# Kernel tuning notes

Hardware: AMD Instinct MI355X
Metric: run time of the kernel (lower is better)

The kernel has to match this reference:

```python
import jax, jax.numpy as jnp
import numpy as np

N_NODES = 100000


def gcn_conv(x, src, dst, ew, W, b, n_nodes):
    """PyG-style GCNConv: add self-loops, symmetric degree normalization,
    linear transform, scatter-add aggregation, bias."""
    loop = jnp.arange(n_nodes)
    src_f = jnp.concatenate([src, loop])          # [E+N]
    dst_f = jnp.concatenate([dst, loop])          # [E+N]
    ew_f = jnp.concatenate([ew, jnp.ones((n_nodes,), dtype=ew.dtype)])
    deg = jax.ops.segment_sum(ew_f, dst_f, num_segments=n_nodes)  # [N]
    dinv = jnp.where(deg > 0, jax.lax.rsqrt(deg), 0.0)
    norm = dinv[src_f] * ew_f * dinv[dst_f]       # [E+N]
    h = x @ W.T                                   # [N, out]
    msg = h[src_f] * norm[:, None]                # [E+N, out] gather + scale
    out = jax.ops.segment_sum(msg, dst_f, num_segments=n_nodes)
    return out + b


def prelu(x, a):
    return jnp.where(x >= 0, x, a * x)


def setup_inputs() -> dict:
    key = jax.random.key(0)
    k = jax.random.split(key, 8)
    in_c, out_c = 256, 128
    n_edges = 1600000
    x = jax.random.normal(k[0], (N_NODES, in_c), dtype=jnp.float32)
    edge_index = jax.random.randint(k[1], (2, n_edges), 0, N_NODES, dtype=jnp.int64)
    edge_weight = jax.random.uniform(k[2], (n_edges,), dtype=jnp.float32)
    W1 = jax.random.normal(k[3], (out_c, in_c), dtype=jnp.float32) / np.sqrt(in_c)
    b1 = jnp.zeros((out_c,), dtype=jnp.float32)
    W2 = jax.random.normal(k[4], (out_c, out_c), dtype=jnp.float32) / np.sqrt(out_c)
    b2 = jnp.zeros((out_c,), dtype=jnp.float32)
    a = jnp.asarray(0.25, dtype=jnp.float32)  # PReLU single shared parameter
    return {"x": x, "edge_index": edge_index, "edge_weight": edge_weight,
            "W1": W1, "b1": b1, "W2": W2, "b2": b2, "a": a}


def reference(x, edge_index, edge_weight, W1, b1, W2, b2, a):
    src, dst = edge_index[0], edge_index[1]
    h1 = prelu(gcn_conv(x, src, dst, edge_weight, W1, b1, N_NODES), a)
    h2 = prelu(gcn_conv(h1, src, dst, edge_weight, W2, b2, N_NODES), a)
    return (h1, h2)
```

## Files before the change

kernel.cpp:

```cpp
#include <hip/hip_runtime.h>


static __device__ __forceinline__ float4 ld4(const float* p) { return *(const float4*)p; }

static __device__ __forceinline__ unsigned short f2bf(float f) {
    unsigned u = __float_as_uint(f);
    u += 0x7fff + ((u >> 16) & 1);
    return (unsigned short)(u >> 16);
}
static __device__ __forceinline__ float bf2f(unsigned short h) {
    return __uint_as_float(((unsigned)h) << 16);
}

typedef __attribute__((ext_vector_type(8))) short short8v;
typedef __attribute__((ext_vector_type(4))) float f32x4;

static __device__ __forceinline__ int eidx(const void* ei, int flag, long long idx) {
    if (flag) return (int)((const long long*)ei)[idx];
    return ((const int*)ei)[idx];
}

#define CNT_SH 24
#define DEG_SCALE 262144.0f
#define DEG_INV   3.814697265625e-06f

__global__ void k_detect(const int* ei, int* flag) {
    __shared__ int anynz;
    if (threadIdx.x == 0) anynz = 0;
    __syncthreads();
    if (ei[2 * threadIdx.x + 1] != 0) anynz = 1;
    __syncthreads();
    if (threadIdx.x == 0) *flag = (anynz == 0) ? 1 : 0;
}

static __device__ __forceinline__ void packW_body(const float* __restrict__ W,
                                                  unsigned short* __restrict__ Bp,
                                                  int t, int kbits) {
    int K = 1 << kbits;
    int col = t >> kbits, k = t & (K - 1);
    int nt = col >> 4, ks = k >> 5;
    int lane = (col & 15) | (((k >> 3) & 3) << 4);
    int j = k & 7;
    Bp[((((size_t)nt * (K >> 5) + ks) * 64 + lane) << 3) + j] = f2bf(W[t]);
}

__global__ __launch_bounds__(256) void k_prep(unsigned* __restrict__ packed, int N,
                                              const float* __restrict__ W1,
                                              unsigned short* __restrict__ bp1,
                                              const float* __restrict__ W2,
                                              unsigned short* __restrict__ bp2,
                                              int nbInit) {
    int b = blockIdx.x;
    if (b < nbInit) {
        int i = b * 256 + threadIdx.x;
        if (i < N) packed[i] = 0u;
    } else if (b < nbInit + 128) {
        int t = (b - nbInit) * 256 + threadIdx.x;
        packW_body(W1, bp1, t, 8);
    } else {
        int t = (b - nbInit - 128) * 256 + threadIdx.x;
        packW_body(W2, bp2, t, 7);
    }
}

static __device__ __forceinline__ void count_body(const void* __restrict__ ei,
                                                  const float* __restrict__ ew,
                                                  int flag,
                                                  unsigned* __restrict__ packed,
                                                  int* __restrict__ rank,
                                                  int E, int cbid) {
    int base = cbid * 2048 + threadIdx.x;
    int d[8]; unsigned inc[8];
    #pragma unroll
    for (int u = 0; u < 8; ++u) {
        int e = base + u * 256;
        bool ok = e < E;
        int ec = ok ? e : 0;
        d[u]   = eidx(ei, flag, (long long)E + ec);
        inc[u] = ok ? ((1u << CNT_SH) | (unsigned)(ew[ec] * DEG_SCALE)) : 0u;
    }
    unsigned old[8];
    #pragma unroll
    for (int u = 0; u < 8; ++u)
        old[u] = atomicAdd(&packed[d[u]], inc[u]);
    __builtin_amdgcn_sched_barrier(0);
    #pragma unroll
    for (int u = 0; u < 8; ++u) {
        int e = base + u * 256;
        if (e < E) rank[e] = (int)(old[u] >> CNT_SH);
    }
}

template <int K>
static __device__ __forceinline__ void gemm_body(const float* __restrict__ X,
                                                 const unsigned short* __restrict__ Bp,
                                                 unsigned short* __restrict__ Hb,
                                                 int M, int gbid) {
    constexpr int KS = K / 32;
    int wave = threadIdx.x >> 6, lane = threadIdx.x & 63;
    int row0 = gbid * 128 + wave * 32;
    int r0 = row0 + (lane & 15);      if (r0 >= M) r0 = M - 1;
    int r1 = row0 + 16 + (lane & 15); if (r1 >= M) r1 = M - 1;
    int kc = (lane >> 4) * 8;
    const float* x0 = X + (size_t)r0 * K + kc;
    const float* x1 = X + (size_t)r1 * K + kc;

    f32x4 acc[2][8] = {};
    #pragma unroll 2
    for (int ks = 0; ks < KS; ++ks) {
        float4 a0 = ld4(x0 + ks * 32), a1 = ld4(x0 + ks * 32 + 4);
        float4 c0 = ld4(x1 + ks * 32), c1 = ld4(x1 + ks * 32 + 4);
        short8v af0, af1;
        af0[0] = (short)f2bf(a0.x); af0[1] = (short)f2bf(a0.y);
        af0[2] = (short)f2bf(a0.z); af0[3] = (short)f2bf(a0.w);
        af0[4] = (short)f2bf(a1.x); af0[5] = (short)f2bf(a1.y);
        af0[6] = (short)f2bf(a1.z); af0[7] = (short)f2bf(a1.w);
        af1[0] = (short)f2bf(c0.x); af1[1] = (short)f2bf(c0.y);
        af1[2] = (short)f2bf(c0.z); af1[3] = (short)f2bf(c0.w);
        af1[4] = (short)f2bf(c1.x); af1[5] = (short)f2bf(c1.y);
        af1[6] = (short)f2bf(c1.z); af1[7] = (short)f2bf(c1.w);
        #pragma unroll
        for (int nt = 0; nt < 8; ++nt) {
            short8v bf = *(const short8v*)&Bp[(((size_t)nt * KS + ks) * 64 + lane) * 8];
            acc[0][nt] = __builtin_amdgcn_mfma_f32_16x16x32_bf16(af0, bf, acc[0][nt], 0, 0, 0);
            acc[1][nt] = __builtin_amdgcn_mfma_f32_16x16x32_bf16(af1, bf, acc[1][nt], 0, 0, 0);
        }
    }
    #pragma unroll
    for (int rg = 0; rg < 2; ++rg) {
        int orow0 = row0 + rg * 16 + (lane >> 4) * 4;
        #pragma unroll
        for (int nt = 0; nt < 8; ++nt) {
            int col = nt * 16 + (lane & 15);
            #pragma unroll
            for (int j = 0; j < 4; ++j) {
                int r = orow0 + j;
                if (r < M) Hb[(size_t)r * 128 + col] = f2bf(acc[rg][nt][j]);
            }
        }
    }
}

__global__ __launch_bounds__(256) void k_count_gemm1(
        const void* __restrict__ ei, const float* __restrict__ ew,
        const int* __restrict__ flagp, unsigned* __restrict__ packed,
        int* __restrict__ rank, int E,
        const float* __restrict__ X, const unsigned short* __restrict__ Bp,
        unsigned short* __restrict__ Hb, int M, int nbCount) {
    int b = blockIdx.x;
    if (b < nbCount) {
        count_body(ei, ew, *flagp, packed, rank, E, b);
    } else {
        gemm_body<256>(X, Bp, Hb, M, b - nbCount);
    }
}

__global__ __launch_bounds__(256) void k_gemm2(const float* __restrict__ X,
                                               const unsigned short* __restrict__ Bp,
                                               unsigned short* __restrict__ Hb, int M) {
    gemm_body<128>(X, Bp, Hb, M, blockIdx.x);
}

__global__ __launch_bounds__(256) void k_blocksum(const unsigned* packed,
                                                  int* bsum, int N) {
    int i = blockIdx.x * 256 + threadIdx.x;
    int v = i < N ? (int)(packed[i] >> CNT_SH) : 0;
    for (int d = 32; d > 0; d >>= 1) v += __shfl_down(v, d, 64);
    __shared__ int wsum[4];
    int lane = threadIdx.x & 63, wid = threadIdx.x >> 6;
    if (lane == 0) wsum[wid] = v;
    __syncthreads();
    if (threadIdx.x == 0) bsum[blockIdx.x] = wsum[0] + wsum[1] + wsum[2] + wsum[3];
}

__global__ __launch_bounds__(512) void k_scan_bsum(int* bsum, int nb) {
    int t = threadIdx.x;
    int v = (t < nb) ? bsum[t] : 0;
    int orig = v;
    int lane = t & 63, wid = t >> 6;
    for (int d = 1; d < 64; d <<= 1) { int n = __shfl_up(v, d, 64); if (lane >= d) v += n; }
    __shared__ int wsum[8];
    if (lane == 63) wsum[wid] = v;
    __syncthreads();
    int woff = 0;
    for (int w = 0; w < 8; ++w) if (w < wid) woff += wsum[w];
    if (t < nb) bsum[t] = v - orig + woff;
}

__global__ __launch_bounds__(256) void k_scan_final(const unsigned* packed,
                                                    const int* bsum,
                                                    int* offs, float* dinv,
                                                    int N, int E) {
    int b = blockIdx.x, t = threadIdx.x;
    int i = b * 256 + t;
    unsigned pk = (i < N) ? packed[i] : 0u;
    int v = (int)(pk >> CNT_SH);
    int orig = v;
    int lane = t & 63, wid = t >> 6;
    for (int d = 1; d < 64; d <<= 1) { int n = __shfl_up(v, d, 64); if (lane >= d) v += n; }
    __shared__ int wsum[4];
    if (lane == 63) wsum[wid] = v;
    __syncthreads();
    int woff = bsum[b];
    for (int w = 0; w < 4; ++w) if (w < wid) woff += wsum[w];
    if (i < N) {
        offs[i] = v - orig + woff;
        float dg = 1.0f + (float)(pk & 0xFFFFFFu) * DEG_INV;
        dinv[i] = rsqrtf(dg);
    }
    if (i == 0) offs[N] = E;
}

__global__ __launch_bounds__(256) void k_scatter(const void* __restrict__ ei,
                                                 const float* __restrict__ ew,
                                                 const int* __restrict__ flagp,
                                                 const float* __restrict__ dinv,
                                                 const int* __restrict__ offs,
                                                 const int* __restrict__ rank,
                                                 int2* __restrict__ spair, int E) {
    const int flag = *flagp;
    int e = blockIdx.x * 256 + threadIdx.x;
    if (e < E) {
        int s = eidx(ei, flag, e);
        int d = eidx(ei, flag, (long long)E + e);
        int p = offs[d] + rank[e];
        float nrm = dinv[s] * ew[e] * dinv[d];
        int2 v; v.x = s; v.y = __float_as_int(nrm);
        spair[p] = v;
    }
}

__global__ __launch_bounds__(256) void k_agg(const unsigned short* __restrict__ Hb,
                                             const int* __restrict__ offs,
                                             const int2* __restrict__ spair,
                                             const float* __restrict__ dinv,
                                             const float* __restrict__ bias,
                                             const float* __restrict__ a_ptr,
                                             float* __restrict__ Out, int N) {
    int g = blockIdx.x * 8 + (threadIdx.x >> 5);
    int lane = threadIdx.x & 31;
    if (g >= N) return;
    float alpha = a_ptr[0];
    float di = dinv[g];
    float4 acc = ld4(bias + lane * 4);
    ushort4 hv = *(const ushort4*)(Hb + (size_t)g * 128 + lane * 4);
    float sw = di * di;
    acc.x += bf2f(hv.x) * sw; acc.y += bf2f(hv.y) * sw;
    acc.z += bf2f(hv.z) * sw; acc.w += bf2f(hv.w) * sw;
    int j0 = offs[g], j1 = offs[g + 1];
    for (int jb = j0; jb < j1; jb += 32) {
        int j = jb + lane;
        int s = 0; float w = 0.f;
        if (j < j1) { int2 sp = spair[j]; s = sp.x; w = __int_as_float(sp.y); }
        int cnt = j1 - jb; if (cnt > 32) cnt = 32;
        int full = cnt & ~3, i = 0;
        for (; i < full; i += 4) {
            int   s0 = __shfl(s, i,     32), s1 = __shfl(s, i + 1, 32);
            int   s2 = __shfl(s, i + 2, 32), s3 = __shfl(s, i + 3, 32);
            float w0 = __shfl(w, i,     32), w1 = __shfl(w, i + 1, 32);
            float w2 = __shfl(w, i + 2, 32), w3 = __shfl(w, i + 3, 32);
            ushort4 h0 = *(const ushort4*)(Hb + (size_t)s0 * 128 + lane * 4);
            ushort4 h1 = *(const ushort4*)(Hb + (size_t)s1 * 128 + lane * 4);
            ushort4 h2 = *(const ushort4*)(Hb + (size_t)s2 * 128 + lane * 4);
            ushort4 h3 = *(const ushort4*)(Hb + (size_t)s3 * 128 + lane * 4);
            acc.x += bf2f(h0.x) * w0; acc.y += bf2f(h0.y) * w0;
            acc.z += bf2f(h0.z) * w0; acc.w += bf2f(h0.w) * w0;
            acc.x += bf2f(h1.x) * w1; acc.y += bf2f(h1.y) * w1;
            acc.z += bf2f(h1.z) * w1; acc.w += bf2f(h1.w) * w1;
            acc.x += bf2f(h2.x) * w2; acc.y += bf2f(h2.y) * w2;
            acc.z += bf2f(h2.z) * w2; acc.w += bf2f(h2.w) * w2;
            acc.x += bf2f(h3.x) * w3; acc.y += bf2f(h3.y) * w3;
            acc.z += bf2f(h3.z) * w3; acc.w += bf2f(h3.w) * w3;
        }
        for (; i < cnt; ++i) {
            int   sv = __shfl(s, i, 32);
            float wv = __shfl(w, i, 32);
            ushort4 h4 = *(const ushort4*)(Hb + (size_t)sv * 128 + lane * 4);
            acc.x += bf2f(h4.x) * wv; acc.y += bf2f(h4.y) * wv;
            acc.z += bf2f(h4.z) * wv; acc.w += bf2f(h4.w) * wv;
        }
    }
    acc.x = acc.x >= 0.f ? acc.x : alpha * acc.x;
    acc.y = acc.y >= 0.f ? acc.y : alpha * acc.y;
    acc.z = acc.z >= 0.f ? acc.z : alpha * acc.z;
    acc.w = acc.w >= 0.f ? acc.w : alpha * acc.w;
    *(float4*)(Out + (size_t)g * 128 + lane * 4) = acc;
}

extern "C" void kernel_launch(void* const* d_in, const int* in_sizes, int n_in,
                              void* d_out, int out_size, void* d_ws, size_t ws_size,
                              hipStream_t stream) {
    const float* x  = (const float*)d_in[0];
    const void*  ei = d_in[1];
    const float* ew = (const float*)d_in[2];
    const float* W1 = (const float*)d_in[3];
    const float* b1 = (const float*)d_in[4];
    const float* W2 = (const float*)d_in[5];
    const float* b2 = (const float*)d_in[6];
    const float* ap = (const float*)d_in[7];
    const int N = in_sizes[0] / 256;
    const int E = in_sizes[2];

    float* out1 = (float*)d_out;
    float* out2 = out1 + (size_t)N * 128;

    char* p = (char*)d_ws;
    auto alloc = [&](size_t bytes) { void* r = (void*)p; p += (bytes + 255) & ~(size_t)255; return r; };
    unsigned* packed = (unsigned*)alloc((size_t)N * 4);
    float* dinv  = (float*)alloc((size_t)N * 4);
    int*   offs  = (int*)  alloc((size_t)(N + 1) * 4);
    int*   bsum  = (int*)  alloc((size_t)((N + 255) / 256) * 4);
    int*   flag  = (int*)  alloc(256);
    int*   rank  = (int*)  alloc((size_t)E * 4);
    int2*  spair = (int2*) alloc((size_t)E * 8);
    unsigned short* hb  = (unsigned short*)alloc((size_t)N * 128 * 2);
    unsigned short* bp1 = (unsigned short*)alloc((size_t)128 * 256 * 2);
    unsigned short* bp2 = (unsigned short*)alloc((size_t)128 * 128 * 2);

    const int nbN    = (N + 255) / 256;
    const int nbE    = (E + 255) / 256;
    const int nbCnt  = (E + 2047) / 2048;
    const int nbGemm = (N + 127) / 128;

    k_detect<<<1, 256, 0, stream>>>((const int*)ei, flag);
    k_prep<<<nbN + 128 + 64, 256, 0, stream>>>(packed, N, W1, bp1, W2, bp2, nbN);
    k_count_gemm1<<<nbCnt + nbGemm, 256, 0, stream>>>(ei, ew, flag, packed, rank, E,
                                                      x, bp1, hb, N, nbCnt);
    k_blocksum<<<nbN, 256, 0, stream>>>(packed, bsum, N);
    k_scan_bsum<<<1, 512, 0, stream>>>(bsum, nbN);
    k_scan_final<<<nbN, 256, 0, stream>>>(packed, bsum, offs, dinv, N, E);
    k_scatter<<<nbE, 256, 0, stream>>>(ei, ew, flag, dinv, offs, rank, spair, E);

    k_agg<<<(N + 7) / 8, 256, 0, stream>>>(hb, offs, spair, dinv, b1, ap, out1, N);
    k_gemm2<<<nbGemm, 256, 0, stream>>>(out1, bp2, hb, N);
    k_agg<<<(N + 7) / 8, 256, 0, stream>>>(hb, offs, spair, dinv, b2, ap, out2, N);
}
```

Measured before the change: 315.8 us.

## Split fused count/GEMM1 kernel and software-prefetch X loads in GEMM

Splits the combined edge-count and first GEMM kernel into two separate launches, so each kernel gets its own register allocation and the count blocks no longer carry the GEMM's register pressure. The GEMM loop now fully unrolls and prefetches the next K-slice of X into registers while the current slice is converted to bf16 and fed to MFMA. In exchange it adds one kernel launch, loses the concurrency between count and GEMM blocks, and raises register use for the prefetch buffers.

```diff
diff --git a/kernel.cpp b/kernel.cpp
--- a/kernel.cpp
+++ b/kernel.cpp
@@ -63,13 +63,13 @@
     }
 }
 
-static __device__ __forceinline__ void count_body(const void* __restrict__ ei,
-                                                  const float* __restrict__ ew,
-                                                  int flag,
-                                                  unsigned* __restrict__ packed,
-                                                  int* __restrict__ rank,
-                                                  int E, int cbid) {
-    int base = cbid * 2048 + threadIdx.x;
+__global__ __launch_bounds__(256) void k_count(const void* __restrict__ ei,
+                                               const float* __restrict__ ew,
+                                               const int* __restrict__ flagp,
+                                               unsigned* __restrict__ packed,
+                                               int* __restrict__ rank, int E) {
+    const int flag = *flagp;
+    int base = blockIdx.x * 2048 + threadIdx.x;
     int d[8]; unsigned inc[8];
     #pragma unroll
     for (int u = 0; u < 8; ++u) {
@@ -106,10 +106,17 @@
     const float* x1 = X + (size_t)r1 * K + kc;
 
     f32x4 acc[2][8] = {};
-    #pragma unroll 2
+    float4 a0 = ld4(x0),     a1 = ld4(x0 + 4);
+    float4 c0 = ld4(x1),     c1 = ld4(x1 + 4);
+    #pragma unroll
     for (int ks = 0; ks < KS; ++ks) {
-        float4 a0 = ld4(x0 + ks * 32), a1 = ld4(x0 + ks * 32 + 4);
-        float4 c0 = ld4(x1 + ks * 32), c1 = ld4(x1 + ks * 32 + 4);
+        float4 na0, na1, nc0, nc1;
+        if (ks + 1 < KS) {
+            const float* p0 = x0 + (ks + 1) * 32;
+            const float* p1 = x1 + (ks + 1) * 32;
+            na0 = ld4(p0); na1 = ld4(p0 + 4);
+            nc0 = ld4(p1); nc1 = ld4(p1 + 4);
+        }
         short8v af0, af1;
         af0[0] = (short)f2bf(a0.x); af0[1] = (short)f2bf(a0.y);
         af0[2] = (short)f2bf(a0.z); af0[3] = (short)f2bf(a0.w);
@@ -125,6 +132,7 @@
             acc[0][nt] = __builtin_amdgcn_mfma_f32_16x16x32_bf16(af0, bf, acc[0][nt], 0, 0, 0);
             acc[1][nt] = __builtin_amdgcn_mfma_f32_16x16x32_bf16(af1, bf, acc[1][nt], 0, 0, 0);
         }
+        a0 = na0; a1 = na1; c0 = nc0; c1 = nc1;
     }
     #pragma unroll
     for (int rg = 0; rg < 2; ++rg) {
@@ -141,18 +149,10 @@
     }
 }
 
-__global__ __launch_bounds__(256) void k_count_gemm1(
-        const void* __restrict__ ei, const float* __restrict__ ew,
-        const int* __restrict__ flagp, unsigned* __restrict__ packed,
-        int* __restrict__ rank, int E,
-        const float* __restrict__ X, const unsigned short* __restrict__ Bp,
-        unsigned short* __restrict__ Hb, int M, int nbCount) {
-    int b = blockIdx.x;
-    if (b < nbCount) {
-        count_body(ei, ew, *flagp, packed, rank, E, b);
-    } else {
-        gemm_body<256>(X, Bp, Hb, M, b - nbCount);
-    }
+__global__ __launch_bounds__(256) void k_gemm1(const float* __restrict__ X,
+                                               const unsigned short* __restrict__ Bp,
+                                               unsigned short* __restrict__ Hb, int M) {
+    gemm_body<256>(X, Bp, Hb, M, blockIdx.x);
 }
 
 __global__ __launch_bounds__(256) void k_gemm2(const float* __restrict__ X,
@@ -324,8 +324,8 @@
 
     k_detect<<<1, 256, 0, stream>>>((const int*)ei, flag);
     k_prep<<<nbN + 128 + 64, 256, 0, stream>>>(packed, N, W1, bp1, W2, bp2, nbN);
-    k_count_gemm1<<<nbCnt + nbGemm, 256, 0, stream>>>(ei, ew, flag, packed, rank, E,
-                                                      x, bp1, hb, N, nbCnt);
+    k_count<<<nbCnt, 256, 0, stream>>>(ei, ew, flag, packed, rank, E);
+    k_gemm1<<<nbGemm, 256, 0, stream>>>(x, bp1, hb, N);
     k_blocksum<<<nbN, 256, 0, stream>>>(packed, bsum, N);
     k_scan_bsum<<<1, 512, 0, stream>>>(bsum, nbN);
     k_scan_final<<<nbN, 256, 0, stream>>>(packed, bsum, offs, dinv, N, E);
```

After: 330.6 us. +4.7%, slower.
